# Kernel optimization log

Measured on AMD Instinct MI355X. Metric: run time of the kernel, lower is better.

Reference implementation:

```python
import jax, jax.numpy as jnp
import numpy as np

NUM_LINKS = 1048576


def _euler_rots(theta):
    # theta: [N,3] -> per-link rotation R = Rz @ Ry @ Rx, shape [N,3,3]
    cx, cy, cz = jnp.cos(theta[:, 0]), jnp.cos(theta[:, 1]), jnp.cos(theta[:, 2])
    sx, sy, sz = jnp.sin(theta[:, 0]), jnp.sin(theta[:, 1]), jnp.sin(theta[:, 2])
    z = jnp.zeros_like(cx)
    o = jnp.ones_like(cx)
    rx = jnp.stack([jnp.stack([o, z, z], -1),
                    jnp.stack([z, cx, -sx], -1),
                    jnp.stack([z, sx, cx], -1)], -2)
    ry = jnp.stack([jnp.stack([cy, z, sy], -1),
                    jnp.stack([z, o, z], -1),
                    jnp.stack([-sy, z, cy], -1)], -2)
    rz = jnp.stack([jnp.stack([cz, -sz, z], -1),
                    jnp.stack([sz, cz, z], -1),
                    jnp.stack([z, z, o], -1)], -2)
    return jnp.matmul(rz, jnp.matmul(ry, rx))  # [N,3,3]


def setup_inputs() -> dict:
    key = jax.random.key(0)
    k1, k2 = jax.random.split(key)
    link_lengths = jax.random.uniform(k1, (NUM_LINKS,), dtype=jnp.float32)
    theta = jax.random.normal(k2, (NUM_LINKS, 3), dtype=jnp.float32)
    return {"link_lengths": link_lengths, "theta": theta}


def reference(link_lengths, theta):
    # Original loop computes eff_pos_i = sum_{j=0..i} (R_0 @ R_1 @ ... @ R_j) @ t_j
    # with t_j = l_j * e_z. Vectorize via prefix matrix products + cumsum.
    R = _euler_rots(theta)                                   # [N,3,3]
    P = jax.lax.associative_scan(jnp.matmul, R)              # P_j = R_0@...@R_j
    v = P[:, :, 2] * link_lengths[:, None]                   # P_j @ (l_j * e_z)
    return jnp.cumsum(v, axis=0)                             # [N,3]
```

## Files before the change

kernel.cpp:

```cpp
#include <hip/hip_runtime.h>
#include <math.h>


#define K1_TPB 512
#define K1_EPT 2
#define K1_EPB (K1_TPB * K1_EPT)
#define K1_NW (K1_TPB / 64)
#define K2_TPB 256
#define K2_EPT 4
#define K2_EPB (K2_TPB * K2_EPT)
#define MAXB 1024
#define EPG (MAXB / K2_TPB)

struct Xf {
    float m[9];
    float p[3];
};

__device__ __forceinline__ void xf_identity(Xf& x) {
    x.m[0] = 1.f; x.m[1] = 0.f; x.m[2] = 0.f;
    x.m[3] = 0.f; x.m[4] = 1.f; x.m[5] = 0.f;
    x.m[6] = 0.f; x.m[7] = 0.f; x.m[8] = 1.f;
    x.p[0] = 0.f; x.p[1] = 0.f; x.p[2] = 0.f;
}

__device__ __forceinline__ Xf xf_comb(const Xf& A, const Xf& B) {
    Xf o;
#pragma unroll
    for (int r = 0; r < 3; ++r) {
        const float a0 = A.m[r * 3 + 0], a1 = A.m[r * 3 + 1], a2 = A.m[r * 3 + 2];
#pragma unroll
        for (int c = 0; c < 3; ++c) {
            o.m[r * 3 + c] = a0 * B.m[0 * 3 + c] + a1 * B.m[1 * 3 + c] + a2 * B.m[2 * 3 + c];
        }
        o.p[r] = A.p[r] + a0 * B.p[0] + a1 * B.p[1] + a2 * B.p[2];
    }
    return o;
}

__device__ __forceinline__ void xf_fold(Xf& a, float ax, float ay, float az, float l) {
    float sx, cx, sy, cy, sz, cz;
    sincosf(ax, &sx, &cx);
    sincosf(ay, &sy, &cy);
    sincosf(az, &sz, &cz);
    const float sysx = sy * sx, sycx = sy * cx;
    const float r00 = cz * cy;
    const float r01 = cz * sysx - sz * cx;
    const float r02 = sz * sx + cz * sycx;
    const float r10 = sz * cy;
    const float r11 = cz * cx + sz * sysx;
    const float r12 = sz * sycx - cz * sx;
    const float r20 = -sy;
    const float r21 = cy * sx;
    const float r22 = cy * cx;
    const float t0 = l * r02, t1 = l * r12, t2 = l * r22;
    const float p0 = a.p[0] + a.m[0] * t0 + a.m[1] * t1 + a.m[2] * t2;
    const float p1 = a.p[1] + a.m[3] * t0 + a.m[4] * t1 + a.m[5] * t2;
    const float p2 = a.p[2] + a.m[6] * t0 + a.m[7] * t1 + a.m[8] * t2;
    const float n0 = a.m[0] * r00 + a.m[1] * r10 + a.m[2] * r20;
    const float n1 = a.m[0] * r01 + a.m[1] * r11 + a.m[2] * r21;
    const float n2 = a.m[0] * r02 + a.m[1] * r12 + a.m[2] * r22;
    const float n3 = a.m[3] * r00 + a.m[4] * r10 + a.m[5] * r20;
    const float n4 = a.m[3] * r01 + a.m[4] * r11 + a.m[5] * r21;
    const float n5 = a.m[3] * r02 + a.m[4] * r12 + a.m[5] * r22;
    const float n6 = a.m[6] * r00 + a.m[7] * r10 + a.m[8] * r20;
    const float n7 = a.m[6] * r01 + a.m[7] * r11 + a.m[8] * r21;
    const float n8 = a.m[6] * r02 + a.m[7] * r12 + a.m[8] * r22;
    a.m[0] = n0; a.m[1] = n1; a.m[2] = n2;
    a.m[3] = n3; a.m[4] = n4; a.m[5] = n5;
    a.m[6] = n6; a.m[7] = n7; a.m[8] = n8;
    a.p[0] = p0; a.p[1] = p1; a.p[2] = p2;
}

__device__ __forceinline__ Xf xf_shfl_up(const Xf& a, int delta) {
    Xf o;
#pragma unroll
    for (int k = 0; k < 9; ++k) o.m[k] = __shfl_up(a.m[k], delta, 64);
#pragma unroll
    for (int k = 0; k < 3; ++k) o.p[k] = __shfl_up(a.p[k], delta, 64);
    return o;
}
__device__ __forceinline__ Xf xf_shfl_down(const Xf& a, int delta) {
    Xf o;
#pragma unroll
    for (int k = 0; k < 9; ++k) o.m[k] = __shfl_down(a.m[k], delta, 64);
#pragma unroll
    for (int k = 0; k < 3; ++k) o.p[k] = __shfl_down(a.p[k], delta, 64);
    return o;
}

__device__ __forceinline__ Xf wave_scan(Xf a, int lane) {
#pragma unroll
    for (int off = 1; off < 64; off <<= 1) {
        const Xf b = xf_shfl_up(a, off);
        if (lane >= off) a = xf_comb(b, a);
    }
    return a;
}

__device__ __forceinline__ Xf wave_reduce(Xf v, int lane) {
#pragma unroll
    for (int off = 1; off < 64; off <<= 1) {
        const Xf b = xf_shfl_down(v, off);
        if (lane + off < 64) v = xf_comb(v, b);
    }
    return v;
}

__device__ __forceinline__ Xf xf_load4(const Xf* p) {
    const float4* g = (const float4*)p;
    const float4 x = g[0], y = g[1], z = g[2];
    Xf b;
    b.m[0] = x.x; b.m[1] = x.y; b.m[2] = x.z;
    b.m[3] = x.w; b.m[4] = y.x; b.m[5] = y.y;
    b.m[6] = y.z; b.m[7] = y.w; b.m[8] = z.x;
    b.p[0] = z.y; b.p[1] = z.z; b.p[2] = z.w;
    return b;
}
__device__ __forceinline__ void xf_store4(Xf* p, const Xf& b) {
    float4* g = (float4*)p;
    g[0] = make_float4(b.m[0], b.m[1], b.m[2], b.m[3]);
    g[1] = make_float4(b.m[4], b.m[5], b.m[6], b.m[7]);
    g[2] = make_float4(b.m[8], b.p[0], b.p[1], b.p[2]);
}

__device__ __forceinline__ void xf_apply(const Xf& T, float q0, float q1, float q2,
                                         float& o0, float& o1, float& o2) {
    o0 = T.p[0] + T.m[0] * q0 + T.m[1] * q1 + T.m[2] * q2;
    o1 = T.p[1] + T.m[3] * q0 + T.m[4] * q1 + T.m[5] * q2;
    o2 = T.p[2] + T.m[6] * q0 + T.m[7] * q1 + T.m[8] * q2;
}

__global__ void __launch_bounds__(K1_TPB, 6)
fk_local(const float* __restrict__ ll, const float* __restrict__ th,
         Xf* __restrict__ agg, float* __restrict__ out, int n) {
    __shared__ Xf wagg[K1_NW];
    const int t = threadIdx.x, bid = blockIdx.x;
    const int lane = t & 63, w = t >> 6;
    const long long j0 = (long long)bid * K1_EPB + (long long)t * K1_EPT;

    Xf a;
    xf_identity(a);
    float pe[K1_EPT][3];
    if (j0 + K1_EPT <= n) {
        const float2* th2 = (const float2*)(th + 3 * j0);
        const float2 d0 = th2[0], d1 = th2[1], d2 = th2[2];
        const float2 L = *(const float2*)(ll + j0);
        xf_fold(a, d0.x, d0.y, d1.x, L.x);
        pe[0][0] = a.p[0]; pe[0][1] = a.p[1]; pe[0][2] = a.p[2];
        xf_fold(a, d1.y, d2.x, d2.y, L.y);
        pe[1][0] = a.p[0]; pe[1][1] = a.p[1]; pe[1][2] = a.p[2];
    } else {
#pragma unroll
        for (int e = 0; e < K1_EPT; ++e) {
            const long long j = j0 + e;
            if (j < n) xf_fold(a, th[3 * j + 0], th[3 * j + 1], th[3 * j + 2], ll[j]);
            pe[e][0] = a.p[0]; pe[e][1] = a.p[1]; pe[e][2] = a.p[2];
        }
    }

    const Xf inc = wave_scan(a, lane);
    if (lane == 63) wagg[w] = inc;
    __syncthreads();

    Xf exw;
    xf_identity(exw);
    for (int k = 0; k < w; ++k) exw = xf_comb(exw, wagg[k]);

    if (t == K1_TPB - 1) xf_store4(&agg[bid], xf_comb(exw, inc));

    const Xf ext = xf_shfl_up(inc, 1);
    Xf T = exw;
    if (lane != 0) T = xf_comb(T, ext);

    if (j0 + K1_EPT <= n) {
        float o0, o1, o2, o3, o4, o5;
        xf_apply(T, pe[0][0], pe[0][1], pe[0][2], o0, o1, o2);
        xf_apply(T, pe[1][0], pe[1][1], pe[1][2], o3, o4, o5);
        float2* q2 = (float2*)(out + 3 * j0);
        q2[0] = make_float2(o0, o1);
        q2[1] = make_float2(o2, o3);
        q2[2] = make_float2(o4, o5);
    } else {
#pragma unroll
        for (int e = 0; e < K1_EPT; ++e) {
            const long long j = j0 + e;
            if (j < n) {
                float o0, o1, o2;
                xf_apply(T, pe[e][0], pe[e][1], pe[e][2], o0, o1, o2);
                out[3 * j + 0] = o0; out[3 * j + 1] = o1; out[3 * j + 2] = o2;
            }
        }
    }
}

__global__ void __launch_bounds__(K2_TPB)
fk_fixup(const Xf* __restrict__ agg, float* __restrict__ out, int n, int nb) {
    __shared__ Xf wred[K2_TPB / 64];
    __shared__ Xf shG;
    const int t = threadIdx.x, bid = blockIdx.x;
    const int lane = t & 63, w = t >> 6;

    {
        const int i0 = t * EPG;
        Xf A;
        xf_identity(A);
#pragma unroll
        for (int e = 0; e < EPG; ++e) {
            const int i = i0 + e;
            if (i < bid) A = xf_comb(A, xf_load4(&agg[i]));
        }
        const Xf red = wave_reduce(A, lane);
        if (lane == 0) wred[w] = red;
    }
    __syncthreads();
    if (t == 0) {
        Xf G = wred[0];
#pragma unroll
        for (int k = 1; k < K2_TPB / 64; ++k) G = xf_comb(G, wred[k]);
        shG = G;
    }
    __syncthreads();
    const Xf G = shG;

    const long long j0 = (long long)bid * K2_EPB + (long long)t * K2_EPT;
    if (j0 + K2_EPT <= n) {
        float4* o4 = (float4*)(out + 3 * j0);
        const float4 x = o4[0], y = o4[1], z = o4[2];
        float r[12];
        xf_apply(G, x.x, x.y, x.z, r[0], r[1], r[2]);
        xf_apply(G, x.w, y.x, y.y, r[3], r[4], r[5]);
        xf_apply(G, y.z, y.w, z.x, r[6], r[7], r[8]);
        xf_apply(G, z.y, z.z, z.w, r[9], r[10], r[11]);
        o4[0] = make_float4(r[0], r[1], r[2], r[3]);
        o4[1] = make_float4(r[4], r[5], r[6], r[7]);
        o4[2] = make_float4(r[8], r[9], r[10], r[11]);
    } else {
#pragma unroll
        for (int e = 0; e < K2_EPT; ++e) {
            const long long j = j0 + e;
            if (j < n) {
                float o0, o1, o2;
                xf_apply(G, out[3 * j + 0], out[3 * j + 1], out[3 * j + 2], o0, o1, o2);
                out[3 * j + 0] = o0; out[3 * j + 1] = o1; out[3 * j + 2] = o2;
            }
        }
    }
}

extern "C" void kernel_launch(void* const* d_in, const int* in_sizes, int n_in,
                              void* d_out, int out_size, void* d_ws, size_t ws_size,
                              hipStream_t stream) {
    const float* ll = (const float*)d_in[0];
    const float* th = (const float*)d_in[1];
    float* out = (float*)d_out;
    const int n = in_sizes[0];

    int nb = (n + K1_EPB - 1) / K1_EPB;
    if (nb > MAXB) nb = MAXB;

    Xf* agg = (Xf*)d_ws;

    fk_local<<<nb, K1_TPB, 0, stream>>>(ll, th, agg, out, n);
    fk_fixup<<<nb, K2_TPB, 0, stream>>>(agg, out, n, nb);
}
```

Before: 29.80 us.

## Fuse local scan and fixup into one cooperative kernel with grid sync

```diff
diff --git a/kernel.cpp b/kernel.cpp
--- a/kernel.cpp
+++ b/kernel.cpp
@@ -1,16 +1,20 @@
 #include <hip/hip_runtime.h>
+#include <hip/hip_cooperative_groups.h>
 #include <math.h>
 
+namespace cg = cooperative_groups;
+
+
+#define TPB 256
+#define EPT 4
+#define EPB (TPB * EPT)
+#define MAXB 1024
+#define NWAVE (TPB / 64)
 
 #define K1_TPB 512
 #define K1_EPT 2
 #define K1_EPB (K1_TPB * K1_EPT)
 #define K1_NW (K1_TPB / 64)
-#define K2_TPB 256
-#define K2_EPT 4
-#define K2_EPB (K2_TPB * K2_EPT)
-#define MAXB 1024
-#define EPG (MAXB / K2_TPB)
 
 struct Xf {
     float m[9];
@@ -38,11 +42,33 @@
     return o;
 }
 
+__device__ __forceinline__ void fast_sincos(float x, float& s, float& c) {
+    const float fn = __builtin_rintf(x * 0.636619772367581343f);
+    const int n = (int)fn;
+    float r = __builtin_fmaf(fn, -1.57079637050628662109375f, x);
+    r = __builtin_fmaf(fn, 4.37113900018624283e-8f, r);
+    const float r2 = r * r;
+    float sp = __builtin_fmaf(r2, -1.9515295891e-4f, 8.3321608736e-3f);
+    sp = __builtin_fmaf(r2, sp, -1.6666654611e-1f);
+    const float ss = __builtin_fmaf(r * r2, sp, r);
+    float cp = __builtin_fmaf(r2, 2.443315711809948e-5f, -1.388731625493765e-3f);
+    cp = __builtin_fmaf(r2, cp, 4.166664568298827e-2f);
+    const float cc = __builtin_fmaf(r2 * r2, cp,
+                                    __builtin_fmaf(r2, -0.5f, 1.0f));
+    const int q = n & 3;
+    const float s0 = (q & 1) ? cc : ss;
+    const float c0 = (q & 1) ? ss : cc;
+    const unsigned sgn_s = (unsigned)(q & 2) << 30;
+    const unsigned sgn_c = (unsigned)((q + 1) & 2) << 30;
+    s = __uint_as_float(__float_as_uint(s0) ^ sgn_s);
+    c = __uint_as_float(__float_as_uint(c0) ^ sgn_c);
+}
+
 __device__ __forceinline__ void xf_fold(Xf& a, float ax, float ay, float az, float l) {
     float sx, cx, sy, cy, sz, cz;
-    sincosf(ax, &sx, &cx);
-    sincosf(ay, &sy, &cy);
-    sincosf(az, &sz, &cz);
+    fast_sincos(ax, sx, cx);
+    fast_sincos(ay, sy, cy);
+    fast_sincos(az, sz, cz);
     const float sysx = sy * sx, sycx = sy * cx;
     const float r00 = cz * cy;
     const float r01 = cz * sysx - sz * cx;
@@ -131,6 +157,122 @@
     o2 = T.p[2] + T.m[6] * q0 + T.m[7] * q1 + T.m[8] * q2;
 }
 
+template <int E>
+__device__ __forceinline__ void local_fold(const float* __restrict__ ll,
+                                           const float* __restrict__ th,
+                                           long long j0, int n, Xf& a,
+                                           float pe[E][3]) {
+    xf_identity(a);
+    if (j0 + E <= n) {
+        if constexpr (E == 4) {
+            const float4* th4 = (const float4*)(th + 3 * j0);
+            const float4 A = th4[0], B = th4[1], C = th4[2];
+            const float4 L = *(const float4*)(ll + j0);
+            xf_fold(a, A.x, A.y, A.z, L.x);
+            pe[0][0] = a.p[0]; pe[0][1] = a.p[1]; pe[0][2] = a.p[2];
+            xf_fold(a, A.w, B.x, B.y, L.y);
+            pe[1][0] = a.p[0]; pe[1][1] = a.p[1]; pe[1][2] = a.p[2];
+            xf_fold(a, B.z, B.w, C.x, L.z);
+            pe[2][0] = a.p[0]; pe[2][1] = a.p[1]; pe[2][2] = a.p[2];
+            xf_fold(a, C.y, C.z, C.w, L.w);
+            pe[3][0] = a.p[0]; pe[3][1] = a.p[1]; pe[3][2] = a.p[2];
+        } else {
+            const float2* th2 = (const float2*)(th + 3 * j0);
+            const float2 d0 = th2[0], d1 = th2[1], d2 = th2[2];
+            const float2 L = *(const float2*)(ll + j0);
+            xf_fold(a, d0.x, d0.y, d1.x, L.x);
+            pe[0][0] = a.p[0]; pe[0][1] = a.p[1]; pe[0][2] = a.p[2];
+            xf_fold(a, d1.y, d2.x, d2.y, L.y);
+            pe[1][0] = a.p[0]; pe[1][1] = a.p[1]; pe[1][2] = a.p[2];
+        }
+    } else {
+#pragma unroll
+        for (int e = 0; e < E; ++e) {
+            const long long j = j0 + e;
+            if (j < n) xf_fold(a, th[3 * j + 0], th[3 * j + 1], th[3 * j + 2], ll[j]);
+            pe[e][0] = a.p[0]; pe[e][1] = a.p[1]; pe[e][2] = a.p[2];
+        }
+    }
+}
+
+__global__ void __launch_bounds__(TPB, 4)
+fk_coop(const float* __restrict__ ll, const float* __restrict__ th,
+        Xf* __restrict__ agg, float* __restrict__ out, int n) {
+    __shared__ Xf wagg[NWAVE];
+    __shared__ Xf shG;
+    const int t = threadIdx.x, bid = blockIdx.x;
+    const int lane = t & 63, w = t >> 6;
+    const long long j0 = (long long)bid * EPB + (long long)t * EPT;
+
+    Xf a;
+    float pe[EPT][3];
+    local_fold<EPT>(ll, th, j0, n, a, pe);
+
+    const Xf inc = wave_scan(a, lane);
+    if (lane == 63) wagg[w] = inc;
+    __syncthreads();
+
+    Xf exw;
+    xf_identity(exw);
+    for (int k = 0; k < w; ++k) exw = xf_comb(exw, wagg[k]);
+
+    if (t == TPB - 1) xf_store4(&agg[bid], xf_comb(exw, inc));
+
+    const Xf ext = xf_shfl_up(inc, 1);
+    Xf T = exw;
+    if (lane != 0) T = xf_comb(T, ext);
+
+    float q[EPT][3];
+#pragma unroll
+    for (int e = 0; e < EPT; ++e)
+        xf_apply(T, pe[e][0], pe[e][1], pe[e][2], q[e][0], q[e][1], q[e][2]);
+
+    cg::this_grid().sync();
+
+    {
+        const int i0 = t * EPT;
+        Xf A;
+        xf_identity(A);
+#pragma unroll
+        for (int e = 0; e < EPT; ++e) {
+            const int i = i0 + e;
+            if (i < bid) A = xf_comb(A, xf_load4(&agg[i]));
+        }
+        const Xf red = wave_reduce(A, lane);
+        if (lane == 0) wagg[w] = red;
+    }
+    __syncthreads();
+    if (t == 0) {
+        Xf G = wagg[0];
+#pragma unroll
+        for (int k = 1; k < NWAVE; ++k) G = xf_comb(G, wagg[k]);
+        shG = G;
+    }
+    __syncthreads();
+    const Xf G = shG;
+
+    if (j0 + EPT <= n) {
+        float o[EPT * 3];
+#pragma unroll
+        for (int e = 0; e < EPT; ++e)
+            xf_apply(G, q[e][0], q[e][1], q[e][2], o[e * 3 + 0], o[e * 3 + 1], o[e * 3 + 2]);
+        float4* o4 = (float4*)(out + 3 * j0);
+        o4[0] = make_float4(o[0], o[1], o[2], o[3]);
+        o4[1] = make_float4(o[4], o[5], o[6], o[7]);
+        o4[2] = make_float4(o[8], o[9], o[10], o[11]);
+    } else {
+#pragma unroll
+        for (int e = 0; e < EPT; ++e) {
+            const long long j = j0 + e;
+            if (j < n) {
+                float o0, o1, o2;
+                xf_apply(G, q[e][0], q[e][1], q[e][2], o0, o1, o2);
+                out[3 * j + 0] = o0; out[3 * j + 1] = o1; out[3 * j + 2] = o2;
+            }
+        }
+    }
+}
+
 __global__ void __launch_bounds__(K1_TPB, 6)
 fk_local(const float* __restrict__ ll, const float* __restrict__ th,
          Xf* __restrict__ agg, float* __restrict__ out, int n) {
@@ -140,24 +282,8 @@
     const long long j0 = (long long)bid * K1_EPB + (long long)t * K1_EPT;
 
     Xf a;
-    xf_identity(a);
     float pe[K1_EPT][3];
-    if (j0 + K1_EPT <= n) {
-        const float2* th2 = (const float2*)(th + 3 * j0);
-        const float2 d0 = th2[0], d1 = th2[1], d2 = th2[2];
-        const float2 L = *(const float2*)(ll + j0);
-        xf_fold(a, d0.x, d0.y, d1.x, L.x);
-        pe[0][0] = a.p[0]; pe[0][1] = a.p[1]; pe[0][2] = a.p[2];
-        xf_fold(a, d1.y, d2.x, d2.y, L.y);
-        pe[1][0] = a.p[0]; pe[1][1] = a.p[1]; pe[1][2] = a.p[2];
-    } else {
-#pragma unroll
-        for (int e = 0; e < K1_EPT; ++e) {
-            const long long j = j0 + e;
-            if (j < n) xf_fold(a, th[3 * j + 0], th[3 * j + 1], th[3 * j + 2], ll[j]);
-            pe[e][0] = a.p[0]; pe[e][1] = a.p[1]; pe[e][2] = a.p[2];
-        }
-    }
+    local_fold<K1_EPT>(ll, th, j0, n, a, pe);
 
     const Xf inc = wave_scan(a, lane);
     if (lane == 63) wagg[w] = inc;
@@ -194,19 +320,19 @@
     }
 }
 
-__global__ void __launch_bounds__(K2_TPB)
+__global__ void __launch_bounds__(TPB)
 fk_fixup(const Xf* __restrict__ agg, float* __restrict__ out, int n, int nb) {
-    __shared__ Xf wred[K2_TPB / 64];
+    __shared__ Xf wred[NWAVE];
     __shared__ Xf shG;
     const int t = threadIdx.x, bid = blockIdx.x;
     const int lane = t & 63, w = t >> 6;
 
     {
-        const int i0 = t * EPG;
+        const int i0 = t * EPT;
         Xf A;
         xf_identity(A);
 #pragma unroll
-        for (int e = 0; e < EPG; ++e) {
+        for (int e = 0; e < EPT; ++e) {
             const int i = i0 + e;
             if (i < bid) A = xf_comb(A, xf_load4(&agg[i]));
         }
@@ -217,14 +343,14 @@
     if (t == 0) {
         Xf G = wred[0];
 #pragma unroll
-        for (int k = 1; k < K2_TPB / 64; ++k) G = xf_comb(G, wred[k]);
+        for (int k = 1; k < NWAVE; ++k) G = xf_comb(G, wred[k]);
         shG = G;
     }
     __syncthreads();
     const Xf G = shG;
 
-    const long long j0 = (long long)bid * K2_EPB + (long long)t * K2_EPT;
-    if (j0 + K2_EPT <= n) {
+    const long long j0 = (long long)bid * EPB + (long long)t * EPT;
+    if (j0 + EPT <= n) {
         float4* o4 = (float4*)(out + 3 * j0);
         const float4 x = o4[0], y = o4[1], z = o4[2];
         float r[12];
@@ -237,7 +363,7 @@
         o4[2] = make_float4(r[8], r[9], r[10], r[11]);
     } else {
 #pragma unroll
-        for (int e = 0; e < K2_EPT; ++e) {
+        for (int e = 0; e < EPT; ++e) {
             const long long j = j0 + e;
             if (j < n) {
                 float o0, o1, o2;
@@ -254,13 +380,20 @@
     const float* ll = (const float*)d_in[0];
     const float* th = (const float*)d_in[1];
     float* out = (float*)d_out;
-    const int n = in_sizes[0];
-
-    int nb = (n + K1_EPB - 1) / K1_EPB;
+    int n = in_sizes[0];
+
+    int nb = (n + EPB - 1) / EPB;
     if (nb > MAXB) nb = MAXB;
 
     Xf* agg = (Xf*)d_ws;
 
-    fk_local<<<nb, K1_TPB, 0, stream>>>(ll, th, agg, out, n);
-    fk_fixup<<<nb, K2_TPB, 0, stream>>>(agg, out, n, nb);
-}
+    void* args[] = {(void*)&ll, (void*)&th, (void*)&agg, (void*)&out, (void*)&n};
+    hipError_t err = hipLaunchCooperativeKernel((const void*)fk_coop, dim3(nb), dim3(TPB),
+                                                args, 0, stream);
+    if (err != hipSuccess) {
+        int nb1 = (n + K1_EPB - 1) / K1_EPB;
+        if (nb1 > MAXB) nb1 = MAXB;
+        fk_local<<<nb1, K1_TPB, 0, stream>>>(ll, th, agg, out, n);
+        fk_fixup<<<nb, TPB, 0, stream>>>(agg, out, n, nb);
+    }
+}
```

After: 95.09 us. 219% more time.
